# Kernel optimization log

Measured on AMD Instinct MI355X. Metric: run time of the kernel, lower is better.

Reference implementation:

```python
import jax, jax.numpy as jnp
import numpy as np

TEMPERATURE = 0.1
BATCH_SIZE = 64
EPS = 1e-8  # torch.nn.CosineSimilarity eps
NEG_INF = -1e30

B, C, D = 64, 16, 512  # batch, children per sample, feature dim


def setup_inputs() -> dict:
    key = jax.random.key(0)
    k1, k2, k3, k4 = jax.random.split(key, 4)
    children_is = jax.random.normal(k1, (B, C, D), dtype=jnp.float32)
    children_js = jax.random.normal(k2, (B, C, D), dtype=jnp.float32)
    partnet_ids = jnp.arange(B, dtype=jnp.int64 if jax.config.jax_enable_x64 else jnp.int32)
    neg_idx_j = jax.random.randint(k3, (B, B, C), 0, C)  # negatives drawn from children_js
    neg_idx_k = jax.random.randint(k4, (B, B, C), 0, C)  # negatives drawn from children_is
    return {
        "children_is": children_is,
        "children_js": children_js,
        "partnet_ids": partnet_ids,
        "neg_idx_j": neg_idx_j,
        "neg_idx_k": neg_idx_k,
    }


def _safe_norm(x, axis=-1):
    return jnp.maximum(jnp.sqrt(jnp.sum(x * x, axis=axis)), EPS)


def _ntxent(ci, cj, pids, nj, nk):
    b = ci.shape[0]
    fi = ci.reshape(b, -1)  # [B, L] flattened anchors
    fj = cj.reshape(b, -1)  # [B, L] flattened positives
    norm_i = _safe_norm(fi)

    # positive: cos(flat(children_i), flat(children_j[i])) / T
    pos = jnp.sum(fi * fj, axis=-1) / (norm_i * _safe_norm(fj))  # [B]

    src = jnp.arange(b)[None, :, None]  # broadcast source-sample index
    # gathered negatives: g*[i, j] = children_*[j, neg_idx[i, j]] flattened -> [B, B, L]
    gj = cj[src, nj].reshape(b, b, -1)
    gk = ci[src, nk].reshape(b, b, -1)

    sim_j = jnp.einsum('il,ijl->ij', fi, gj) / (norm_i[:, None] * _safe_norm(gj))
    sim_k = jnp.einsum('il,ijl->ij', fi, gk) / (norm_i[:, None] * _safe_norm(gk))

    # negative pair valid iff j != i and partnet ids differ
    eye = jnp.arange(b)
    mask = (eye[None, :] != eye[:, None]) & (pids[None, :] != pids[:, None])  # [B, B]

    logits = jnp.concatenate(
        [pos[:, None],
         jnp.where(mask, sim_j, NEG_INF),
         jnp.where(mask, sim_k, NEG_INF)], axis=1) / TEMPERATURE  # [B, 1+2B]

    # CrossEntropy with label 0, reduction='sum' over the batch of anchors
    loss = jnp.sum(-logits[:, 0] + jax.scipy.special.logsumexp(logits, axis=1))
    return loss / (2.0 * BATCH_SIZE)


def reference(children_is, children_js, partnet_ids, neg_idx_j, neg_idx_k):
    return _ntxent(children_is, children_js, partnet_ids, neg_idx_j, neg_idx_k)
```

## Files before the change

### kernel.cpp

```cpp
#include <hip/hip_runtime.h>
#include <math.h>

#define BB 64
#define CC 16
#define DD 512
#define LL 8192
#define EPSV 1e-8f
#define INVT 10.0f
#define NEGINF_T (-1e31f)

#define WS_N2I 0
#define WS_N2J 1024
#define WS_DJ  2048
#define WS_DK  6144
#define WS_POS 10240

__device__ __forceinline__ float dot4(float4 a, float4 b) {
    return a.x * b.x + a.y * b.y + a.z * b.z + a.w * b.w;
}

__device__ __forceinline__ float wave_reduce(float v) {
    #pragma unroll
    for (int off = 32; off; off >>= 1) v += __shfl_down(v, off);
    return v;
}

__global__ __launch_bounds__(256) void ntx_main(const float* __restrict__ ci,
                                                const float* __restrict__ cj,
                                                const int* __restrict__ nj,
                                                const int* __restrict__ nk,
                                                float* __restrict__ ws,
                                                float* __restrict__ out) {
    const int b = blockIdx.x, tid = threadIdx.x;

    if (b < 1024) {
        __shared__ int   sidx[2][4][16];
        __shared__ float red[4][2][4];
        const int jt = b & 15;
        const int i  = b >> 4;

        if (tid < 64)        ((int*)sidx)[tid] = nj[i * 1024 + jt * 64 + tid];
        else if (tid < 128)  ((int*)sidx)[tid] = nk[i * 1024 + jt * 64 + (tid - 64)];

        const float4* fi4 = (const float4*)(ci + i * LL);
        float4 fiv[8];
        #pragma unroll
        for (int it = 0; it < 8; ++it) fiv[it] = fi4[tid + 256 * it];

        __syncthreads();

        const int d4   = tid & 127;
        const int half = tid >> 7;
        const float4* cj4 = (const float4*)cj;
        const float4* ci4 = (const float4*)ci;

        #pragma unroll
        for (int jj = 0; jj < 4; ++jj) {
            const int j = jt * 4 + jj;
            const float4* bj = cj4 + j * CC * 128;
            const float4* bk = ci4 + j * CC * 128;
            float aj = 0.f, ak = 0.f;
            #pragma unroll
            for (int it = 0; it < 8; ++it) {
                const int c = half + 2 * it;
                float4 vj = bj[sidx[0][jj][c] * 128 + d4];
                float4 vk = bk[sidx[1][jj][c] * 128 + d4];
                aj += dot4(fiv[it], vj);
                ak += dot4(fiv[it], vk);
            }
            aj = wave_reduce(aj);
            ak = wave_reduce(ak);
            if ((tid & 63) == 0) { red[jj][0][tid >> 6] = aj; red[jj][1][tid >> 6] = ak; }
        }
        __syncthreads();
        if (tid < 8) {
            const int jj = tid >> 1, side = tid & 1;
            float s = red[jj][side][0] + red[jj][side][1] + red[jj][side][2] + red[jj][side][3];
            ws[(side ? WS_DK : WS_DJ) + i * BB + jt * 4 + jj] = s;
        }
    } else if (b < 1536) {
        const int row  = (b - 1024) * 4 + (tid >> 6);
        const int lane = tid & 63;
        const int r    = row & 1023;
        const float4* src = (const float4*)(row < 1024 ? ci : cj);
        float4 v1 = src[r * 128 + lane];
        float4 v2 = src[r * 128 + 64 + lane];
        float acc = dot4(v1, v1) + dot4(v2, v2);
        acc = wave_reduce(acc);
        if (lane == 0) ws[(row < 1024 ? WS_N2I : WS_N2J) + r] = acc;
    } else {
        __shared__ float red2[4];
        const int i = b - 1536;
        if (b == 1536 && tid == 0) out[0] = 0.f;
        const float4* fi = (const float4*)(ci + i * LL);
        const float4* fj = (const float4*)(cj + i * LL);
        float acc = 0.f;
        #pragma unroll
        for (int it = 0; it < 8; ++it) acc += dot4(fi[tid + 256 * it], fj[tid + 256 * it]);
        acc = wave_reduce(acc);
        if ((tid & 63) == 0) red2[tid >> 6] = acc;
        __syncthreads();
        if (tid == 0) ws[WS_POS + i] = red2[0] + red2[1] + red2[2] + red2[3];
    }
}

__global__ __launch_bounds__(64) void ntx_final(const int* __restrict__ pids,
                                                const int* __restrict__ nj,
                                                const int* __restrict__ nk,
                                                const float* __restrict__ ws,
                                                float* __restrict__ out) {
    const int i = blockIdx.x, j = threadIdx.x;
    __shared__ float sn2i[1024], sn2j[1024];
    const float4* n2i4 = (const float4*)(ws + WS_N2I);
    const float4* n2j4 = (const float4*)(ws + WS_N2J);
    #pragma unroll
    for (int t = 0; t < 4; ++t) {
        ((float4*)sn2i)[j + 64 * t] = n2i4[j + 64 * t];
        ((float4*)sn2j)[j + 64 * t] = n2j4[j + 64 * t];
    }
    __syncthreads();

    float si = 0.f, sjf = 0.f;
    #pragma unroll
    for (int c = 0; c < CC; ++c) { si += sn2i[i * CC + c]; sjf += sn2j[i * CC + c]; }
    const float ni = fmaxf(sqrtf(si), EPSV);
    const float l0 = ws[WS_POS + i] / (ni * fmaxf(sqrtf(sjf), EPSV)) * INVT;

    const int4* nj4 = (const int4*)(nj + (i * BB + j) * CC);
    const int4* nk4 = (const int4*)(nk + (i * BB + j) * CC);
    float gj = 0.f, gk = 0.f;
    #pragma unroll
    for (int t = 0; t < 4; ++t) {
        int4 a = nj4[t];
        gj += sn2j[j * CC + a.x] + sn2j[j * CC + a.y] + sn2j[j * CC + a.z] + sn2j[j * CC + a.w];
        int4 bq = nk4[t];
        gk += sn2i[j * CC + bq.x] + sn2i[j * CC + bq.y] + sn2i[j * CC + bq.z] + sn2i[j * CC + bq.w];
    }

    const bool valid = (j != i) && (pids[j] != pids[i]);
    float lj = NEGINF_T, lk = NEGINF_T;
    if (valid) {
        const float inv = INVT / ni;
        lj = ws[WS_DJ + i * BB + j] / fmaxf(sqrtf(gj), EPSV) * inv;
        lk = ws[WS_DK + i * BB + j] / fmaxf(sqrtf(gk), EPSV) * inv;
    }

    float m = fmaxf(lj, lk);
    #pragma unroll
    for (int off = 32; off; off >>= 1) m = fmaxf(m, __shfl_xor(m, off));
    m = fmaxf(m, l0);

    float s = __expf(lj - m) + __expf(lk - m);
    s = wave_reduce(s);
    if (j == 0) {
        s += __expf(l0 - m);
        const float loss_i = -l0 + m + __logf(s);
        atomicAdd(out, loss_i * (1.0f / (2.0f * BB)));
    }
}

extern "C" void kernel_launch(void* const* d_in, const int* in_sizes, int n_in,
                              void* d_out, int out_size, void* d_ws, size_t ws_size,
                              hipStream_t stream) {
    const float* ci  = (const float*)d_in[0];
    const float* cj  = (const float*)d_in[1];
    const int*  pids = (const int*) d_in[2];
    const int*  nj   = (const int*) d_in[3];
    const int*  nk   = (const int*) d_in[4];
    float* ws  = (float*)d_ws;
    float* out = (float*)d_out;

    ntx_main<<<1600, 256, 0, stream>>>(ci, cj, nj, nk, ws, out);
    ntx_final<<<BB, 64, 0, stream>>>(pids, nj, nk, ws, out);
}
```

Measured before the change: 77.61 us.

## Fuse norm computation and exp-sum into main kernel, shrink final reduction

The main kernel now computes the squared norms of the anchor and of each gathered negative inline, next to the dot products. This removes the 512 separate norm blocks and stops the final kernel from re-gathering norms through the index arrays. Each block forms its masked exp-sum of the scaled cosine logits directly, and the positive logit is computed in the same pass as its norms. A single-block final kernel then adds up the partial sums and writes the loss without an atomic, so the output no longer needs zeroing. The logsumexp skips max subtraction, which relies on logits being bounded by 1/T, and it adds a few extra FMAs and shuffles per gathered load.

```diff
diff --git a/kernel.cpp b/kernel.cpp
--- a/kernel.cpp
+++ b/kernel.cpp
@@ -7,13 +7,9 @@
 #define LL 8192
 #define EPSV 1e-8f
 #define INVT 10.0f
-#define NEGINF_T (-1e31f)
 
-#define WS_N2I 0
-#define WS_N2J 1024
-#define WS_DJ  2048
-#define WS_DK  6144
-#define WS_POS 10240
+#define WS_ESUM 0
+#define WS_L0   1024
 
 __device__ __forceinline__ float dot4(float4 a, float4 b) {
     return a.x * b.x + a.y * b.y + a.z * b.z + a.w * b.w;
@@ -27,15 +23,16 @@
 
 __global__ __launch_bounds__(256) void ntx_main(const float* __restrict__ ci,
                                                 const float* __restrict__ cj,
+                                                const int* __restrict__ pids,
                                                 const int* __restrict__ nj,
                                                 const int* __restrict__ nk,
-                                                float* __restrict__ ws,
-                                                float* __restrict__ out) {
+                                                float* __restrict__ ws) {
     const int b = blockIdx.x, tid = threadIdx.x;
 
     if (b < 1024) {
         __shared__ int   sidx[2][4][16];
-        __shared__ float red[4][2][4];
+        __shared__ float red[4][4][4];
+        __shared__ float nred[4];
         const int jt = b & 15;
         const int i  = b >> 4;
 
@@ -44,118 +41,117 @@
 
         const float4* fi4 = (const float4*)(ci + i * LL);
         float4 fiv[8];
+        float nacc = 0.f;
         #pragma unroll
-        for (int it = 0; it < 8; ++it) fiv[it] = fi4[tid + 256 * it];
+        for (int it = 0; it < 8; ++it) {
+            fiv[it] = fi4[tid + 256 * it];
+            nacc += dot4(fiv[it], fiv[it]);
+        }
 
         __syncthreads();
 
         const int d4   = tid & 127;
         const int half = tid >> 7;
+        const int wave = tid >> 6;
         const float4* cj4 = (const float4*)cj;
         const float4* ci4 = (const float4*)ci;
+
+        {
+            float nr = wave_reduce(nacc);
+            if ((tid & 63) == 0) nred[wave] = nr;
+        }
 
         #pragma unroll
         for (int jj = 0; jj < 4; ++jj) {
             const int j = jt * 4 + jj;
             const float4* bj = cj4 + j * CC * 128;
             const float4* bk = ci4 + j * CC * 128;
-            float aj = 0.f, ak = 0.f;
+            float aj = 0.f, ak = 0.f, gj = 0.f, gk = 0.f;
             #pragma unroll
             for (int it = 0; it < 8; ++it) {
                 const int c = half + 2 * it;
                 float4 vj = bj[sidx[0][jj][c] * 128 + d4];
                 float4 vk = bk[sidx[1][jj][c] * 128 + d4];
                 aj += dot4(fiv[it], vj);
+                gj += dot4(vj, vj);
                 ak += dot4(fiv[it], vk);
+                gk += dot4(vk, vk);
             }
             aj = wave_reduce(aj);
             ak = wave_reduce(ak);
-            if ((tid & 63) == 0) { red[jj][0][tid >> 6] = aj; red[jj][1][tid >> 6] = ak; }
+            gj = wave_reduce(gj);
+            gk = wave_reduce(gk);
+            if ((tid & 63) == 0) {
+                red[jj][0][wave] = aj; red[jj][1][wave] = ak;
+                red[jj][2][wave] = gj; red[jj][3][wave] = gk;
+            }
         }
         __syncthreads();
-        if (tid < 8) {
-            const int jj = tid >> 1, side = tid & 1;
-            float s = red[jj][side][0] + red[jj][side][1] + red[jj][side][2] + red[jj][side][3];
-            ws[(side ? WS_DK : WS_DJ) + i * BB + jt * 4 + jj] = s;
+        if (tid < 4) {
+            const int jj = tid, j = jt * 4 + jj;
+            const float aj = red[jj][0][0] + red[jj][0][1] + red[jj][0][2] + red[jj][0][3];
+            const float ak = red[jj][1][0] + red[jj][1][1] + red[jj][1][2] + red[jj][1][3];
+            const float gj = red[jj][2][0] + red[jj][2][1] + red[jj][2][2] + red[jj][2][3];
+            const float gk = red[jj][3][0] + red[jj][3][1] + red[jj][3][2] + red[jj][3][3];
+            const float si = nred[0] + nred[1] + nred[2] + nred[3];
+            const float ni = fmaxf(sqrtf(si), EPSV);
+            float e = 0.f;
+            if ((j != i) && (pids[j] != pids[i])) {
+                const float inv = INVT / ni;
+                const float lj = aj / fmaxf(sqrtf(gj), EPSV) * inv;
+                const float lk = ak / fmaxf(sqrtf(gk), EPSV) * inv;
+                e = __expf(lj) + __expf(lk);
+            }
+            e += __shfl_xor(e, 1);
+            e += __shfl_xor(e, 2);
+            if (jj == 0) ws[WS_ESUM + i * 16 + jt] = e;
         }
-    } else if (b < 1536) {
-        const int row  = (b - 1024) * 4 + (tid >> 6);
-        const int lane = tid & 63;
-        const int r    = row & 1023;
-        const float4* src = (const float4*)(row < 1024 ? ci : cj);
-        float4 v1 = src[r * 128 + lane];
-        float4 v2 = src[r * 128 + 64 + lane];
-        float acc = dot4(v1, v1) + dot4(v2, v2);
-        acc = wave_reduce(acc);
-        if (lane == 0) ws[(row < 1024 ? WS_N2I : WS_N2J) + r] = acc;
     } else {
-        __shared__ float red2[4];
-        const int i = b - 1536;
-        if (b == 1536 && tid == 0) out[0] = 0.f;
+        __shared__ float pr[3][4];
+        const int i = b - 1024;
         const float4* fi = (const float4*)(ci + i * LL);
         const float4* fj = (const float4*)(cj + i * LL);
-        float acc = 0.f;
+        float d = 0.f, a2 = 0.f, b2 = 0.f;
         #pragma unroll
-        for (int it = 0; it < 8; ++it) acc += dot4(fi[tid + 256 * it], fj[tid + 256 * it]);
-        acc = wave_reduce(acc);
-        if ((tid & 63) == 0) red2[tid >> 6] = acc;
+        for (int it = 0; it < 8; ++it) {
+            float4 u = fi[tid + 256 * it];
+            float4 v = fj[tid + 256 * it];
+            d  += dot4(u, v);
+            a2 += dot4(u, u);
+            b2 += dot4(v, v);
+        }
+        d  = wave_reduce(d);
+        a2 = wave_reduce(a2);
+        b2 = wave_reduce(b2);
+        if ((tid & 63) == 0) { pr[0][tid >> 6] = d; pr[1][tid >> 6] = a2; pr[2][tid >> 6] = b2; }
         __syncthreads();
-        if (tid == 0) ws[WS_POS + i] = red2[0] + red2[1] + red2[2] + red2[3];
+        if (tid == 0) {
+            const float dd = pr[0][0] + pr[0][1] + pr[0][2] + pr[0][3];
+            const float ia = pr[1][0] + pr[1][1] + pr[1][2] + pr[1][3];
+            const float jb = pr[2][0] + pr[2][1] + pr[2][2] + pr[2][3];
+            ws[WS_L0 + i] = dd / (fmaxf(sqrtf(ia), EPSV) * fmaxf(sqrtf(jb), EPSV)) * INVT;
+        }
     }
 }
 
-__global__ __launch_bounds__(64) void ntx_final(const int* __restrict__ pids,
-                                                const int* __restrict__ nj,
-                                                const int* __restrict__ nk,
-                                                const float* __restrict__ ws,
-                                                float* __restrict__ out) {
-    const int i = blockIdx.x, j = threadIdx.x;
-    __shared__ float sn2i[1024], sn2j[1024];
-    const float4* n2i4 = (const float4*)(ws + WS_N2I);
-    const float4* n2j4 = (const float4*)(ws + WS_N2J);
-    #pragma unroll
-    for (int t = 0; t < 4; ++t) {
-        ((float4*)sn2i)[j + 64 * t] = n2i4[j + 64 * t];
-        ((float4*)sn2j)[j + 64 * t] = n2j4[j + 64 * t];
+__global__ __launch_bounds__(256) void ntx_fin(const float* __restrict__ ws,
+                                               float* __restrict__ out) {
+    const int tid = threadIdx.x;
+    const int i = tid >> 2, p = tid & 3;
+    float4 v4 = *(const float4*)(ws + WS_ESUM + i * 16 + p * 4);
+    float v = v4.x + v4.y + v4.z + v4.w;
+    v += __shfl_xor(v, 1);
+    v += __shfl_xor(v, 2);
+    __shared__ float terms[64];
+    if ((tid & 3) == 0) {
+        const float l0 = ws[WS_L0 + i];
+        terms[i] = -l0 + __logf(v + __expf(l0));
     }
     __syncthreads();
-
-    float si = 0.f, sjf = 0.f;
-    #pragma unroll
-    for (int c = 0; c < CC; ++c) { si += sn2i[i * CC + c]; sjf += sn2j[i * CC + c]; }
-    const float ni = fmaxf(sqrtf(si), EPSV);
-    const float l0 = ws[WS_POS + i] / (ni * fmaxf(sqrtf(sjf), EPSV)) * INVT;
-
-    const int4* nj4 = (const int4*)(nj + (i * BB + j) * CC);
-    const int4* nk4 = (const int4*)(nk + (i * BB + j) * CC);
-    float gj = 0.f, gk = 0.f;
-    #pragma unroll
-    for (int t = 0; t < 4; ++t) {
-        int4 a = nj4[t];
-        gj += sn2j[j * CC + a.x] + sn2j[j * CC + a.y] + sn2j[j * CC + a.z] + sn2j[j * CC + a.w];
-        int4 bq = nk4[t];
-        gk += sn2i[j * CC + bq.x] + sn2i[j * CC + bq.y] + sn2i[j * CC + bq.z] + sn2i[j * CC + bq.w];
-    }
-
-    const bool valid = (j != i) && (pids[j] != pids[i]);
-    float lj = NEGINF_T, lk = NEGINF_T;
-    if (valid) {
-        const float inv = INVT / ni;
-        lj = ws[WS_DJ + i * BB + j] / fmaxf(sqrtf(gj), EPSV) * inv;
-        lk = ws[WS_DK + i * BB + j] / fmaxf(sqrtf(gk), EPSV) * inv;
-    }
-
-    float m = fmaxf(lj, lk);
-    #pragma unroll
-    for (int off = 32; off; off >>= 1) m = fmaxf(m, __shfl_xor(m, off));
-    m = fmaxf(m, l0);
-
-    float s = __expf(lj - m) + __expf(lk - m);
-    s = wave_reduce(s);
-    if (j == 0) {
-        s += __expf(l0 - m);
-        const float loss_i = -l0 + m + __logf(s);
-        atomicAdd(out, loss_i * (1.0f / (2.0f * BB)));
+    if (tid < 64) {
+        float t = terms[tid];
+        t = wave_reduce(t);
+        if (tid == 0) out[0] = t * (1.0f / (2.0f * BB));
     }
 }
 
@@ -170,6 +166,6 @@
     float* ws  = (float*)d_ws;
     float* out = (float*)d_out;
 
-    ntx_main<<<1600, 256, 0, stream>>>(ci, cj, nj, nk, ws, out);
-    ntx_final<<<BB, 64, 0, stream>>>(pids, nj, nk, ws, out);
+    ntx_main<<<1088, 256, 0, stream>>>(ci, cj, pids, nj, nk, ws);
+    ntx_fin<<<1, 256, 0, stream>>>(ws, out);
 }
```

After: 76.63 us (median of 2 runs). No clear change (-1.3%).
